# Performance work log

Hardware: AMD Instinct MI355X
Metric: run time of the kernel (lower is better)

The kernel has to match this reference:

```python
import jax, jax.numpy as jnp
import numpy as np

M_IN, N_OUT = 64, 64   # crossbar rows (inputs) x columns (outputs)
BATCH = 256
PARASITIC_R = 2.0      # line + source resistance (ohms)
R_LRS = 1000.0         # low-resistance state -> mapping_coefficient = 1/R_LRS


def _build_abcd(G, g_in, g_out, g_line):
    """Assemble the 2mn x 2mn Kirchhoff system [A B; C D] of memtorch solve_passive.

    Unknowns: V_A (word-line node voltages, index n*i+j) and V_B (bit-line node
    voltages, index n*i+j). Rows of the C/D blocks are indexed j*m+i as in memtorch.
    """
    m, n = G.shape
    mn = m * n
    ii, jj = np.meshgrid(np.arange(m), np.arange(n), indexing='ij')
    ii = ii.ravel(); jj = jj.ravel()
    k = n * ii + jj                      # word-line node flat index
    Gf = G.ravel()
    S = jnp.zeros((2 * mn, 2 * mn), dtype=G.dtype)

    # --- A block (word-line KCL) ---
    diagA = Gf + g_line * ((jj > 0).astype(G.dtype) + (jj < n - 1).astype(G.dtype)) \
            + g_in * (jj == 0).astype(G.dtype)
    S = S.at[k, k].add(diagA)
    kh = k[jj < n - 1]                   # horizontal neighbors along word line
    S = S.at[kh, kh + 1].add(-g_line)
    S = S.at[kh + 1, kh].add(-g_line)

    # --- B block: -G on the (word-line row, bit-line col) diagonal ---
    S = S.at[k, mn + k].add(-Gf)

    # --- C block: +G, rows indexed j*m+i, cols indexed n*i+j ---
    rC = mn + jj * m + ii
    S = S.at[rC, k].add(Gf)

    # --- D block (bit-line KCL), rows j*m+i, cols mn + n*i+j ---
    diagD = -Gf - g_line * ((ii > 0).astype(G.dtype) + (ii < m - 1).astype(G.dtype)) \
            - g_out * (ii == m - 1).astype(G.dtype)
    S = S.at[rC, mn + k].add(diagD)
    sel_dn = ii < m - 1                  # vertical neighbors along bit line
    S = S.at[rC[sel_dn], mn + n * (ii[sel_dn] + 1) + jj[sel_dn]].add(g_line)
    sel_up = ii > 0
    S = S.at[rC[sel_up], mn + n * (ii[sel_up] - 1) + jj[sel_up]].add(g_line)
    return S


def _solve_passive(G, x, g_in, g_out, g_line):
    """Batched crossbar circuit solve. G:(m,n), x:(B,m) -> column currents (B,n)."""
    m, n = G.shape
    mn = m * n
    ABCD = _build_abcd(G, g_in, g_out, g_line)
    # RHS: applied word-line voltages enter at node j=0 of each row; V_BL = 0.
    E = jnp.zeros((2 * mn, x.shape[0]), dtype=x.dtype)
    E = E.at[np.arange(m) * n, :].set(g_in * x.T)
    V = jnp.linalg.solve(ABCD, E)        # (2mn, B), one factorization for all batches
    VA = V[:mn].reshape(m, n, -1)
    VB = V[mn:].reshape(m, n, -1)
    I = ((VA - VB) * G[:, :, None]).sum(axis=0)   # column output currents (n, B)
    return I.T


def setup_inputs() -> dict:
    key = jax.random.key(0)
    kx, kw, kb = jax.random.split(key, 3)
    x = jax.random.uniform(kx, (BATCH, M_IN), dtype=jnp.float32)
    weight = jax.random.uniform(kw, (N_OUT, M_IN), dtype=jnp.float32)
    bias = jax.random.normal(kb, (N_OUT,), dtype=jnp.float32)
    return {"x": x, "weight": weight, "bias": bias}


def reference(x, weight, bias):
    c = 1.0 / R_LRS                      # mapping_coefficient
    g = 1.0 / PARASITIC_R                # g_source = g_line (module passes same R twice)
    G = weight.T * c                     # (m_in, n_out) conductance matrix
    currents = _solve_passive(G, x, g, g, g)   # (B, n_out)
    return currents / c + bias
```

## Files before the change

kernel.cpp:

```cpp
#include <hip/hip_runtime.h>

#define SP 65
#define A_SZ (64*SP)
#define SPL 65
#define NT 1024
#define NBIT 4

#define OFF_G    0
#define OFF_U    (OFF_G + A_SZ)
#define OFF_W    (OFF_U + 128*SPL)
#define OFF_ZM   (OFF_W + 128*SPL)
#define OFF_PR   (OFF_ZM + 2*A_SZ)
#define LDS_FLOATS (OFF_PR + 128)

template<int CTRL>
__device__ __forceinline__ float dpp0(float v) {
    return __builtin_bit_cast(float,
        __builtin_amdgcn_update_dpp(0, __builtin_bit_cast(int, v), CTRL, 0xF, 0xF, true));
}
__device__ __forceinline__ float rdlane(float v, int l) {
    return __builtin_bit_cast(float, __builtin_amdgcn_readlane(__builtin_bit_cast(int, v), l));
}

struct ScanMasks { float p1, p2, p3, s1, s2, s3; };

__device__ __forceinline__ float tri_apply(float r, float su_, float sw_, const ScanMasks& m) {
    float av = su_*r, bv = sw_*r;
    float pa = av;
    pa += dpp0<0x111>(pa);
    pa += dpp0<0x112>(pa);
    pa += dpp0<0x114>(pa);
    pa += dpp0<0x118>(pa);
    pa = __fmaf_rn(m.p1, rdlane(pa,15),
         __fmaf_rn(m.p2, rdlane(pa,31),
         __fmaf_rn(m.p3, rdlane(pa,47), pa)));
    float sb = bv;
    sb += dpp0<0x101>(sb);
    sb += dpp0<0x102>(sb);
    sb += dpp0<0x104>(sb);
    sb += dpp0<0x108>(sb);
    sb = __fmaf_rn(m.s1, rdlane(sb,16),
         __fmaf_rn(m.s2, rdlane(sb,32),
         __fmaf_rn(m.s3, rdlane(sb,48), sb)));
    return sw_*(pa - av) + su_*sb;
}

extern "C" __global__ __launch_bounds__(NT)
void solve_k(const float* __restrict__ Wm, float* __restrict__ Kout) {
    extern __shared__ float lds[];
    float* Gt = lds + OFF_G;
    float* Ul = lds + OFF_U;
    float* Wl = lds + OFF_W;
    float* zm = lds + OFF_ZM;
    float* pr = lds + OFF_PR;

    const int t = threadIdx.x;
    const int wv = t >> 6, lane = t & 63;
    const float gl = 0.5f, gin = 0.5f, gout = 0.5f, c2 = 0.25f;

    for (int s = t; s < 4096; s += NT) {
        int j = s >> 6, i = s & 63;
        Gt[j*SP + i] = Wm[s] * 1e-3f;
    }
    __syncthreads();

    if (t < 128) {
        const int line = t; const bool word = line < 64; const int lc = word ? line : line - 64;
        float Ui = 1.0f, prod = 1.0f, rdprev = 0.f;
        for (int k = 0; k < 64; ++k) {
            float g = word ? Gt[k*SP + lc] : Gt[lc*SP + k];
            float b = g + gl*((k>0)+(k<63)) + (word ? (k==0?gin:0.f) : (k==63?gout:0.f));
            float d = b - c2*rdprev;
            Ul[line*SPL + k] = Ui;
            float rd = __builtin_amdgcn_rcpf(d);
            Ui   *= d*2.0f;
            prod *= 0.5f*rd;
            rdprev = rd;
        }
        pr[line] = prod;
    } else if (t < 256) {
        const int line = t - 128; const bool word = line < 64; const int lc = word ? line : line - 64;
        float Wj = 2.0f, eprev = 0.f;
        for (int k = 63; k >= 0; --k) {
            float g = word ? Gt[k*SP + lc] : Gt[lc*SP + k];
            float b = g + gl*((k>0)+(k<63)) + (word ? (k==0?gin:0.f) : (k==63?gout:0.f));
            if (k == 63) { Wl[line*SPL + 63] = Wj; eprev = b; }
            else {
                Wj *= eprev*2.0f;
                Wl[line*SPL + k] = Wj;
                eprev = b - c2*__builtin_amdgcn_rcpf(eprev);
            }
        }
    }
    __syncthreads();

    float su[8], swt[8], gsg[8];
    #pragma unroll
    for (int li = 0; li < 4; ++li) {
        const int L = wv*4 + li;
        su[li]    = Ul[L*SPL + lane];
        swt[li]   = Wl[L*SPL + lane] * pr[L];
        gsg[li]   = Gt[lane*SP + L];
        su[4+li]  = Ul[(64+L)*SPL + lane];
        swt[4+li] = Wl[(64+L)*SPL + lane] * pr[64+L];
        gsg[4+li] = Gt[L*SP + lane];
    }

    const int i0 = blockIdx.x;

    #pragma unroll
    for (int li = 0; li < 4; ++li) {
        const int L = wv*4 + li;
        zm[L*SP + lane] = (L == i0) ? gin * swt[li] : 0.f;
    }
    __syncthreads();

    const int rrow = lane >> 4;
    ScanMasks m;
    m.p1 = rrow >= 1 ? 1.f : 0.f;  m.p2 = rrow >= 2 ? 1.f : 0.f;  m.p3 = rrow >= 3 ? 1.f : 0.f;
    m.s1 = rrow <  1 ? 1.f : 0.f;  m.s2 = rrow <  2 ? 1.f : 0.f;  m.s3 = rrow <  3 ? 1.f : 0.f;

    #pragma unroll 1
    for (int sw = 0; sw < NBIT; ++sw) {
        #pragma unroll
        for (int li = 0; li < 4; ++li) {
            const int L = wv*4 + li;
            float rhs = gsg[4+li] * zm[lane*SP + L];
            float vb = tri_apply(rhs, su[4+li], swt[4+li], m);
            if (sw < NBIT-1) {
                zm[A_SZ + lane*SP + L] = vb;
            } else if (lane == 63) {
                Kout[i0*64 + L] = 1000.0f * gout * vb;
            }
        }
        if (sw == NBIT-1) break;
        __syncthreads();

        #pragma unroll
        for (int li = 0; li < 4; ++li) {
            const int L = wv*4 + li;
            float rhs = gsg[li] * zm[A_SZ + L*SP + lane];
            if (L == i0 && lane == 0) rhs += gin;
            zm[L*SP + lane] = tri_apply(rhs, su[li], swt[li], m);
        }
        __syncthreads();
    }
}

extern "C" __global__ __launch_bounds__(256)
void apply_k(const float* __restrict__ X, const float* __restrict__ Kmat,
             const float* __restrict__ bias, float* __restrict__ out) {
    __shared__ float Ks[4096];
    __shared__ float Xs[256];
    __shared__ float Bs[64];
    const int t = threadIdx.x;
    const int b0 = blockIdx.x * 4;

    #pragma unroll
    for (int p = 0; p < 4; ++p)
        *(float4*)&Ks[(p*256 + t)*4] = *(const float4*)&Kmat[(p*256 + t)*4];
    Xs[t] = X[b0*64 + t];
    if (t < 64) Bs[t] = bias[t];
    __syncthreads();

    const int bl = t >> 6, j = t & 63;
    float acc = Bs[j];
    #pragma unroll 8
    for (int i = 0; i < 64; ++i) acc += Xs[bl*64 + i] * Ks[i*64 + j];
    out[(b0 + bl)*64 + j] = acc;
}

extern "C" void kernel_launch(void* const* d_in, const int* in_sizes, int n_in,
                              void* d_out, int out_size, void* d_ws, size_t ws_size,
                              hipStream_t stream) {
    const float* x    = (const float*)d_in[0];
    const float* w    = (const float*)d_in[1];
    const float* bias = (const float*)d_in[2];
    float* out  = (float*)d_out;
    float* Kmat = (float*)d_ws;

    size_t lds_bytes = (size_t)LDS_FLOATS * sizeof(float);
    hipFuncSetAttribute((const void*)solve_k,
                        hipFuncAttributeMaxDynamicSharedMemorySize, (int)lds_bytes);

    solve_k<<<64, NT, lds_bytes, stream>>>(w, Kmat);
    apply_k<<<64, 256, 0, stream>>>(x, Kmat, bias, out);
}
```

Measured before the change: 21.48 us.

## Solve per batch row directly, fusing response and apply kernels

Instead of solving 64 unit-input systems to build a 64x64 response matrix and then multiplying it by X in a second kernel, each block now solves the circuit for one batch sample's input vector and writes the output plus bias directly. This removes the second launch and the workspace round trip. The cost is 256 blocks instead of 64, each repeating the full factorisation setup and the iterative sweeps, so total solve work grows fourfold.

```diff
diff --git a/kernel.cpp b/kernel.cpp
--- a/kernel.cpp
+++ b/kernel.cpp
@@ -11,7 +11,9 @@
 #define OFF_W    (OFF_U + 128*SPL)
 #define OFF_ZM   (OFF_W + 128*SPL)
 #define OFF_PR   (OFF_ZM + 2*A_SZ)
-#define LDS_FLOATS (OFF_PR + 128)
+#define OFF_X    (OFF_PR + 128)
+#define OFF_B    (OFF_X + 64)
+#define LDS_FLOATS (OFF_B + 64)
 
 template<int CTRL>
 __device__ __forceinline__ float dpp0(float v) {
@@ -46,22 +48,28 @@
 }
 
 extern "C" __global__ __launch_bounds__(NT)
-void solve_k(const float* __restrict__ Wm, float* __restrict__ Kout) {
+void fused_solve(const float* __restrict__ X, const float* __restrict__ Wm,
+                 const float* __restrict__ bias, float* __restrict__ out) {
     extern __shared__ float lds[];
     float* Gt = lds + OFF_G;
     float* Ul = lds + OFF_U;
     float* Wl = lds + OFF_W;
     float* zm = lds + OFF_ZM;
     float* pr = lds + OFF_PR;
+    float* xs = lds + OFF_X;
+    float* bs = lds + OFF_B;
 
     const int t = threadIdx.x;
     const int wv = t >> 6, lane = t & 63;
+    const int b = blockIdx.x;
     const float gl = 0.5f, gin = 0.5f, gout = 0.5f, c2 = 0.25f;
 
     for (int s = t; s < 4096; s += NT) {
         int j = s >> 6, i = s & 63;
         Gt[j*SP + i] = Wm[s] * 1e-3f;
     }
+    if (t < 64) xs[t] = X[b*64 + t];
+    else if (t < 128) bs[t-64] = bias[t-64];
     __syncthreads();
 
     if (t < 128) {
@@ -69,8 +77,8 @@
         float Ui = 1.0f, prod = 1.0f, rdprev = 0.f;
         for (int k = 0; k < 64; ++k) {
             float g = word ? Gt[k*SP + lc] : Gt[lc*SP + k];
-            float b = g + gl*((k>0)+(k<63)) + (word ? (k==0?gin:0.f) : (k==63?gout:0.f));
-            float d = b - c2*rdprev;
+            float bb = g + gl*((k>0)+(k<63)) + (word ? (k==0?gin:0.f) : (k==63?gout:0.f));
+            float d = bb - c2*rdprev;
             Ul[line*SPL + k] = Ui;
             float rd = __builtin_amdgcn_rcpf(d);
             Ui   *= d*2.0f;
@@ -83,18 +91,18 @@
         float Wj = 2.0f, eprev = 0.f;
         for (int k = 63; k >= 0; --k) {
             float g = word ? Gt[k*SP + lc] : Gt[lc*SP + k];
-            float b = g + gl*((k>0)+(k<63)) + (word ? (k==0?gin:0.f) : (k==63?gout:0.f));
-            if (k == 63) { Wl[line*SPL + 63] = Wj; eprev = b; }
+            float bb = g + gl*((k>0)+(k<63)) + (word ? (k==0?gin:0.f) : (k==63?gout:0.f));
+            if (k == 63) { Wl[line*SPL + 63] = Wj; eprev = bb; }
             else {
                 Wj *= eprev*2.0f;
                 Wl[line*SPL + k] = Wj;
-                eprev = b - c2*__builtin_amdgcn_rcpf(eprev);
+                eprev = bb - c2*__builtin_amdgcn_rcpf(eprev);
             }
         }
     }
     __syncthreads();
 
-    float su[8], swt[8], gsg[8];
+    float su[8], swt[8], gsg[8], xr[4];
     #pragma unroll
     for (int li = 0; li < 4; ++li) {
         const int L = wv*4 + li;
@@ -104,14 +112,13 @@
         su[4+li]  = Ul[(64+L)*SPL + lane];
         swt[4+li] = Wl[(64+L)*SPL + lane] * pr[64+L];
         gsg[4+li] = Gt[L*SP + lane];
+        xr[li]    = gin * xs[L];
     }
-
-    const int i0 = blockIdx.x;
 
     #pragma unroll
     for (int li = 0; li < 4; ++li) {
         const int L = wv*4 + li;
-        zm[L*SP + lane] = (L == i0) ? gin * swt[li] : 0.f;
+        zm[L*SP + lane] = xr[li] * swt[li];
     }
     __syncthreads();
 
@@ -130,7 +137,7 @@
             if (sw < NBIT-1) {
                 zm[A_SZ + lane*SP + L] = vb;
             } else if (lane == 63) {
-                Kout[i0*64 + L] = 1000.0f * gout * vb;
+                out[b*64 + L] = 1000.0f * gout * vb + bs[L];
             }
         }
         if (sw == NBIT-1) break;
@@ -140,34 +147,11 @@
         for (int li = 0; li < 4; ++li) {
             const int L = wv*4 + li;
             float rhs = gsg[li] * zm[A_SZ + L*SP + lane];
-            if (L == i0 && lane == 0) rhs += gin;
+            if (lane == 0) rhs += xr[li];
             zm[L*SP + lane] = tri_apply(rhs, su[li], swt[li], m);
         }
         __syncthreads();
     }
-}
-
-extern "C" __global__ __launch_bounds__(256)
-void apply_k(const float* __restrict__ X, const float* __restrict__ Kmat,
-             const float* __restrict__ bias, float* __restrict__ out) {
-    __shared__ float Ks[4096];
-    __shared__ float Xs[256];
-    __shared__ float Bs[64];
-    const int t = threadIdx.x;
-    const int b0 = blockIdx.x * 4;
-
-    #pragma unroll
-    for (int p = 0; p < 4; ++p)
-        *(float4*)&Ks[(p*256 + t)*4] = *(const float4*)&Kmat[(p*256 + t)*4];
-    Xs[t] = X[b0*64 + t];
-    if (t < 64) Bs[t] = bias[t];
-    __syncthreads();
-
-    const int bl = t >> 6, j = t & 63;
-    float acc = Bs[j];
-    #pragma unroll 8
-    for (int i = 0; i < 64; ++i) acc += Xs[bl*64 + i] * Ks[i*64 + j];
-    out[(b0 + bl)*64 + j] = acc;
 }
 
 extern "C" void kernel_launch(void* const* d_in, const int* in_sizes, int n_in,
@@ -177,12 +161,10 @@
     const float* w    = (const float*)d_in[1];
     const float* bias = (const float*)d_in[2];
     float* out  = (float*)d_out;
-    float* Kmat = (float*)d_ws;
 
     size_t lds_bytes = (size_t)LDS_FLOATS * sizeof(float);
-    hipFuncSetAttribute((const void*)solve_k,
+    hipFuncSetAttribute((const void*)fused_solve,
                         hipFuncAttributeMaxDynamicSharedMemorySize, (int)lds_bytes);
 
-    solve_k<<<64, NT, lds_bytes, stream>>>(w, Kmat);
-    apply_k<<<64, 256, 0, stream>>>(x, Kmat, bias, out);
+    fused_solve<<<256, NT, lds_bytes, stream>>>(x, w, bias, out);
 }
```

Measured after the change: 19.24 us. 1.12x faster.
